# Kernel optimization log

Hardware: AMD Instinct MI355X
Metric: run time of the kernel (lower is better)

Reference implementation:

```python
import jax, jax.numpy as jnp
import numpy as np

HEAD_DIM = 64  # d_model // n_heads = 1024 // 16

def setup_inputs() -> dict:
    key = jax.random.key(0)
    k1, k2, k3, k4, k5 = jax.random.split(key, 5)
    B, H, S, D = 4, 16, 1024, HEAD_DIM
    return {
        "q": jax.random.normal(k1, (B, H, S, D), dtype=jnp.float32),
        "k": jax.random.normal(k2, (B, H, D, S), dtype=jnp.float32),
        "v": jax.random.normal(k3, (B, H, S, D), dtype=jnp.float32),
        "prev": jax.random.normal(k4, (B, H, S, S), dtype=jnp.float32),
        "attn_mask": jax.random.normal(k5, (1, 1, S, S), dtype=jnp.float32),
        "scale": jnp.asarray(HEAD_DIM ** (-0.5), dtype=jnp.float32),
    }

def reference(q, k, v, prev, attn_mask, scale):
    # scores: [B, H, S, S]; k is pre-transposed to [B, H, D, S]
    attn_scores = jnp.einsum('bhsd,bhdt->bhst', q, k) * scale
    attn_scores = attn_scores + prev + attn_mask  # additive float mask branch
    attn_weights = jax.nn.softmax(attn_scores, axis=-1)
    # dropout p=0.0 -> identity
    output = jnp.einsum('bhst,bhtd->bhsd', attn_weights, v)
    # res_attention=True -> return scores too
    return (output, attn_weights, attn_scores)
```

## Files before the change

### kernel.cpp

```cpp
#include <hip/hip_runtime.h>

#define S 1024
#define D 64
#define R 16
#define BH 64
#define SUBP 68

typedef float v4f __attribute__((ext_vector_type(4)));

__global__ __launch_bounds__(256, 4)
void attn_fused_kernel(const float* __restrict__ q,
                       const float* __restrict__ k,
                       const float* __restrict__ v,
                       const float* __restrict__ prev,
                       const float* __restrict__ mask,
                       const float* __restrict__ scale_p,
                       float* __restrict__ out,
                       float* __restrict__ weights,
                       float* __restrict__ scores)
{
    __shared__ float q_lds[R][D];
    __shared__ float s_sub[4][R][SUBP];
    __shared__ float red_max[4][R];
    __shared__ float red_sum[4][R];

    const int tile = blockIdx.x;
    const int bh   = blockIdx.y;
    const int tid  = (int)threadIdx.x;
    const int lane = tid & 63;
    const int wid  = tid >> 6;
    const int r0   = tile * R;

    const float* qb = q    + (size_t)bh * S * D + (size_t)r0 * D;
    const float* kb = k    + (size_t)bh * D * S;
    const float* vb = v    + (size_t)bh * S * D;
    const float* pb = prev + (size_t)bh * S * S + (size_t)r0 * S;
    const float* mb = mask + (size_t)r0 * S;
    float* wout = weights + (size_t)bh * S * S + (size_t)r0 * S;
    float* sout = scores  + (size_t)bh * S * S + (size_t)r0 * S;
    float* oout = out     + (size_t)bh * S * D + (size_t)r0 * D;

    const float scale  = *scale_p;
    const float rscale = 1.0f / scale;

    {
        float4 qv = *(const float4*)(qb + (size_t)tid * 4);
        *(float4*)&q_lds[tid >> 4][(tid & 15) * 4] = qv;
    }
    __syncthreads();

    const int t0 = tid * 4;
    float acc[R][4];

#pragma unroll
    for (int r = 0; r < R; ++r) {
        v4f p4 = __builtin_nontemporal_load((const v4f*)(pb + (size_t)r * S + t0));
        v4f m4 = *(const v4f*)(mb + (size_t)r * S + t0);
        acc[r][0] = (p4[0] + m4[0]) * rscale;
        acc[r][1] = (p4[1] + m4[1]) * rscale;
        acc[r][2] = (p4[2] + m4[2]) * rscale;
        acc[r][3] = (p4[3] + m4[3]) * rscale;
    }

#pragma unroll 2
    for (int kk = 0; kk < D / 4; ++kk) {
        const float* kp = kb + (size_t)(kk * 4) * S + t0;
        float4 k0 = *(const float4*)(kp);
        float4 k1 = *(const float4*)(kp + S);
        float4 k2 = *(const float4*)(kp + 2 * S);
        float4 k3 = *(const float4*)(kp + 3 * S);
#pragma unroll
        for (int r = 0; r < R; ++r) {
            float4 q4 = *(const float4*)&q_lds[r][kk * 4];
            acc[r][0] = fmaf(q4.w, k3.x, fmaf(q4.z, k2.x, fmaf(q4.y, k1.x, fmaf(q4.x, k0.x, acc[r][0]))));
            acc[r][1] = fmaf(q4.w, k3.y, fmaf(q4.z, k2.y, fmaf(q4.y, k1.y, fmaf(q4.x, k0.y, acc[r][1]))));
            acc[r][2] = fmaf(q4.w, k3.z, fmaf(q4.z, k2.z, fmaf(q4.y, k1.z, fmaf(q4.x, k0.z, acc[r][2]))));
            acc[r][3] = fmaf(q4.w, k3.w, fmaf(q4.z, k2.w, fmaf(q4.y, k1.w, fmaf(q4.x, k0.w, acc[r][3]))));
        }
    }

#pragma unroll
    for (int r = 0; r < R; ++r) {
        acc[r][0] *= scale; acc[r][1] *= scale; acc[r][2] *= scale; acc[r][3] *= scale;
        v4f s4v = { acc[r][0], acc[r][1], acc[r][2], acc[r][3] };
        __builtin_nontemporal_store(s4v, (v4f*)(sout + (size_t)r * S + t0));
    }

    {
        float rmax[R];
#pragma unroll
        for (int r = 0; r < R; ++r) {
            float m = fmaxf(fmaxf(acc[r][0], acc[r][1]), fmaxf(acc[r][2], acc[r][3]));
#pragma unroll
            for (int off = 32; off > 0; off >>= 1)
                m = fmaxf(m, __shfl_xor(m, off));
            rmax[r] = m;
        }
        if (lane == 0) {
#pragma unroll
            for (int r = 0; r < R; ++r) red_max[wid][r] = rmax[r];
        }
    }
    __syncthreads();

    {
        float rsum[R];
#pragma unroll
        for (int r = 0; r < R; ++r) {
            float gm = fmaxf(fmaxf(red_max[0][r], red_max[1][r]),
                             fmaxf(red_max[2][r], red_max[3][r]));
            acc[r][0] = __expf(acc[r][0] - gm);
            acc[r][1] = __expf(acc[r][1] - gm);
            acc[r][2] = __expf(acc[r][2] - gm);
            acc[r][3] = __expf(acc[r][3] - gm);
            float ssum = (acc[r][0] + acc[r][1]) + (acc[r][2] + acc[r][3]);
#pragma unroll
            for (int off = 32; off > 0; off >>= 1)
                ssum += __shfl_xor(ssum, off);
            rsum[r] = ssum;
        }
        if (lane == 0) {
#pragma unroll
            for (int r = 0; r < R; ++r) red_sum[wid][r] = rsum[r];
        }
    }
    __syncthreads();

#pragma unroll
    for (int r = 0; r < R; ++r) {
        float gs = (red_sum[0][r] + red_sum[1][r]) + (red_sum[2][r] + red_sum[3][r]);
        float inv = 1.0f / gs;
        acc[r][0] *= inv; acc[r][1] *= inv; acc[r][2] *= inv; acc[r][3] *= inv;
        v4f w4v = { acc[r][0], acc[r][1], acc[r][2], acc[r][3] };
        __builtin_nontemporal_store(w4v, (v4f*)(wout + (size_t)r * S + t0));
    }

    const int g0 = lane >> 4;
    const int dq = lane & 15;
    const float* vw = vb + (size_t)(wid * 256) * D;

    float4 p0 = {0.f,0.f,0.f,0.f};
    float4 p1 = {0.f,0.f,0.f,0.f};
    float4 p2 = {0.f,0.f,0.f,0.f};
    float4 p3 = {0.f,0.f,0.f,0.f};

#pragma unroll 1
    for (int s4 = 0; s4 < 4; ++s4) {
        asm volatile("" ::: "memory");
        if (g0 == s4) {
#pragma unroll
            for (int r = 0; r < R; ++r) {
                float4 w4 = { acc[r][0], acc[r][1], acc[r][2], acc[r][3] };
                *(float4*)&s_sub[wid][r][dq * 4] = w4;
            }
        }
        asm volatile("s_waitcnt lgkmcnt(0)" ::: "memory");

        const float* vs = vw + (size_t)(s4 * 64) * D;
#pragma unroll 2
        for (int j = 0; j < 16; ++j) {
            float4 w0 = *(const float4*)&s_sub[wid][g0     ][j * 4];
            float4 w1 = *(const float4*)&s_sub[wid][g0 + 4 ][j * 4];
            float4 w2 = *(const float4*)&s_sub[wid][g0 + 8 ][j * 4];
            float4 w3 = *(const float4*)&s_sub[wid][g0 + 12][j * 4];
            const float* vp = vs + (size_t)(j * 4) * D + dq * 4;
            float4 v0 = *(const float4*)(vp);
            float4 v1 = *(const float4*)(vp + D);
            float4 v2 = *(const float4*)(vp + 2 * D);
            float4 v3 = *(const float4*)(vp + 3 * D);
            p0.x = fmaf(w0.w, v3.x, fmaf(w0.z, v2.x, fmaf(w0.y, v1.x, fmaf(w0.x, v0.x, p0.x))));
            p0.y = fmaf(w0.w, v3.y, fmaf(w0.z, v2.y, fmaf(w0.y, v1.y, fmaf(w0.x, v0.y, p0.y))));
            p0.z = fmaf(w0.w, v3.z, fmaf(w0.z, v2.z, fmaf(w0.y, v1.z, fmaf(w0.x, v0.z, p0.z))));
            p0.w = fmaf(w0.w, v3.w, fmaf(w0.z, v2.w, fmaf(w0.y, v1.w, fmaf(w0.x, v0.w, p0.w))));
            p1.x = fmaf(w1.w, v3.x, fmaf(w1.z, v2.x, fmaf(w1.y, v1.x, fmaf(w1.x, v0.x, p1.x))));
            p1.y = fmaf(w1.w, v3.y, fmaf(w1.z, v2.y, fmaf(w1.y, v1.y, fmaf(w1.x, v0.y, p1.y))));
            p1.z = fmaf(w1.w, v3.z, fmaf(w1.z, v2.z, fmaf(w1.y, v1.z, fmaf(w1.x, v0.z, p1.z))));
            p1.w = fmaf(w1.w, v3.w, fmaf(w1.z, v2.w, fmaf(w1.y, v1.w, fmaf(w1.x, v0.w, p1.w))));
            p2.x = fmaf(w2.w, v3.x, fmaf(w2.z, v2.x, fmaf(w2.y, v1.x, fmaf(w2.x, v0.x, p2.x))));
            p2.y = fmaf(w2.w, v3.y, fmaf(w2.z, v2.y, fmaf(w2.y, v1.y, fmaf(w2.x, v0.y, p2.y))));
            p2.z = fmaf(w2.w, v3.z, fmaf(w2.z, v2.z, fmaf(w2.y, v1.z, fmaf(w2.x, v0.z, p2.z))));
            p2.w = fmaf(w2.w, v3.w, fmaf(w2.z, v2.w, fmaf(w2.y, v1.w, fmaf(w2.x, v0.w, p2.w))));
            p3.x = fmaf(w3.w, v3.x, fmaf(w3.z, v2.x, fmaf(w3.y, v1.x, fmaf(w3.x, v0.x, p3.x))));
            p3.y = fmaf(w3.w, v3.y, fmaf(w3.z, v2.y, fmaf(w3.y, v1.y, fmaf(w3.x, v0.y, p3.y))));
            p3.z = fmaf(w3.w, v3.z, fmaf(w3.z, v2.z, fmaf(w3.y, v1.z, fmaf(w3.x, v0.z, p3.z))));
            p3.w = fmaf(w3.w, v3.w, fmaf(w3.z, v2.w, fmaf(w3.y, v1.w, fmaf(w3.x, v0.w, p3.w))));
        }
    }

    asm volatile("" ::: "memory");
    *(float4*)&s_sub[wid][g0     ][dq * 4] = p0;
    *(float4*)&s_sub[wid][g0 + 4 ][dq * 4] = p1;
    *(float4*)&s_sub[wid][g0 + 8 ][dq * 4] = p2;
    *(float4*)&s_sub[wid][g0 + 12][dq * 4] = p3;
    __syncthreads();
    {
        const int row = tid >> 4;
        const int dq2 = tid & 15;
        float4 a0 = *(const float4*)&s_sub[0][row][dq2 * 4];
        float4 a1 = *(const float4*)&s_sub[1][row][dq2 * 4];
        float4 a2 = *(const float4*)&s_sub[2][row][dq2 * 4];
        float4 a3 = *(const float4*)&s_sub[3][row][dq2 * 4];
        v4f o;
        o[0] = (a0.x + a1.x) + (a2.x + a3.x);
        o[1] = (a0.y + a1.y) + (a2.y + a3.y);
        o[2] = (a0.z + a1.z) + (a2.z + a3.z);
        o[3] = (a0.w + a1.w) + (a2.w + a3.w);
        __builtin_nontemporal_store(o, (v4f*)(oout + (size_t)row * D + dq2 * 4));
    }
}

extern "C" void kernel_launch(void* const* d_in, const int* in_sizes, int n_in,
                              void* d_out, int out_size, void* d_ws, size_t ws_size,
                              hipStream_t stream) {
    (void)in_sizes; (void)n_in; (void)out_size; (void)d_ws; (void)ws_size;
    const float* q     = (const float*)d_in[0];
    const float* k     = (const float*)d_in[1];
    const float* v     = (const float*)d_in[2];
    const float* prev  = (const float*)d_in[3];
    const float* mask  = (const float*)d_in[4];
    const float* scale = (const float*)d_in[5];

    float* out     = (float*)d_out;
    float* weights = out + (size_t)4 * 16 * 1024 * 64;
    float* scores  = weights + (size_t)4 * 16 * 1024 * 1024;

    dim3 grid(S / R, BH);
    attn_fused_kernel<<<grid, 256, 0, stream>>>(q, k, v, prev, mask, scale,
                                                out, weights, scores);
}
```

Before: 377.3 us.

## Halve rows per block and overlap prev/mask loads with the QK loop

Rows per block drop from 16 to 8, with the launch-bounds occupancy hint lowered from 4 to 3, so each thread holds half as many score accumulators and the grid has twice as many blocks. The prev and mask loads move out of a separate prologue and into the first eight iterations of the QK^T loop, so their latency overlaps the K loads and FMAs. The scale and additive bias are then applied afterwards with a single fma per element. The cost is that every K and V tile is now re-read by twice as many blocks, which doubles L2/HBM traffic for those operands.

Result: slower. 430.4 us (+14.1%).

```diff
diff --git a/kernel.cpp b/kernel.cpp
--- a/kernel.cpp
+++ b/kernel.cpp
@@ -2,13 +2,13 @@
 
 #define S 1024
 #define D 64
-#define R 16
+#define R 8
 #define BH 64
 #define SUBP 68
 
 typedef float v4f __attribute__((ext_vector_type(4)));
 
-__global__ __launch_bounds__(256, 4)
+__global__ __launch_bounds__(256, 3)
 void attn_fused_kernel(const float* __restrict__ q,
                        const float* __restrict__ k,
                        const float* __restrict__ v,
@@ -40,10 +40,7 @@
     float* sout = scores  + (size_t)bh * S * S + (size_t)r0 * S;
     float* oout = out     + (size_t)bh * S * D + (size_t)r0 * D;
 
-    const float scale  = *scale_p;
-    const float rscale = 1.0f / scale;
-
-    {
+    if (tid < 128) {
         float4 qv = *(const float4*)(qb + (size_t)tid * 4);
         *(float4*)&q_lds[tid >> 4][(tid & 15) * 4] = qv;
     }
@@ -51,24 +48,22 @@
 
     const int t0 = tid * 4;
     float acc[R][4];
-
 #pragma unroll
     for (int r = 0; r < R; ++r) {
-        v4f p4 = __builtin_nontemporal_load((const v4f*)(pb + (size_t)r * S + t0));
-        v4f m4 = *(const v4f*)(mb + (size_t)r * S + t0);
-        acc[r][0] = (p4[0] + m4[0]) * rscale;
-        acc[r][1] = (p4[1] + m4[1]) * rscale;
-        acc[r][2] = (p4[2] + m4[2]) * rscale;
-        acc[r][3] = (p4[3] + m4[3]) * rscale;
-    }
-
-#pragma unroll 2
-    for (int kk = 0; kk < D / 4; ++kk) {
+        acc[r][0] = 0.f; acc[r][1] = 0.f; acc[r][2] = 0.f; acc[r][3] = 0.f;
+    }
+
+    v4f pbuf[R], mbuf[R];
+
+#pragma unroll
+    for (int kk = 0; kk < 8; ++kk) {
         const float* kp = kb + (size_t)(kk * 4) * S + t0;
         float4 k0 = *(const float4*)(kp);
         float4 k1 = *(const float4*)(kp + S);
         float4 k2 = *(const float4*)(kp + 2 * S);
         float4 k3 = *(const float4*)(kp + 3 * S);
+        pbuf[kk] = __builtin_nontemporal_load((const v4f*)(pb + (size_t)kk * S + t0));
+        mbuf[kk] = *(const v4f*)(mb + (size_t)kk * S + t0);
 #pragma unroll
         for (int r = 0; r < R; ++r) {
             float4 q4 = *(const float4*)&q_lds[r][kk * 4];
@@ -79,9 +74,34 @@
         }
     }
 
+#pragma unroll 2
+    for (int kk = 8; kk < 16; ++kk) {
+        const float* kp = kb + (size_t)(kk * 4) * S + t0;
+        float4 k0 = *(const float4*)(kp);
+        float4 k1 = *(const float4*)(kp + S);
+        float4 k2 = *(const float4*)(kp + 2 * S);
+        float4 k3 = *(const float4*)(kp + 3 * S);
+#pragma unroll
+        for (int r = 0; r < R; ++r) {
+            float4 q4 = *(const float4*)&q_lds[r][kk * 4];
+            acc[r][0] = fmaf(q4.w, k3.x, fmaf(q4.z, k2.x, fmaf(q4.y, k1.x, fmaf(q4.x, k0.x, acc[r][0]))));
+            acc[r][1] = fmaf(q4.w, k3.y, fmaf(q4.z, k2.y, fmaf(q4.y, k1.y, fmaf(q4.x, k0.y, acc[r][1]))));
+            acc[r][2] = fmaf(q4.w, k3.z, fmaf(q4.z, k2.z, fmaf(q4.y, k1.z, fmaf(q4.x, k0.z, acc[r][2]))));
+            acc[r][3] = fmaf(q4.w, k3.w, fmaf(q4.z, k2.w, fmaf(q4.y, k1.w, fmaf(q4.x, k0.w, acc[r][3]))));
+        }
+    }
+
+    const float scale = *scale_p;
 #pragma unroll
     for (int r = 0; r < R; ++r) {
-        acc[r][0] *= scale; acc[r][1] *= scale; acc[r][2] *= scale; acc[r][3] *= scale;
+        float b0 = pbuf[r][0] + mbuf[r][0];
+        float b1 = pbuf[r][1] + mbuf[r][1];
+        float b2 = pbuf[r][2] + mbuf[r][2];
+        float b3 = pbuf[r][3] + mbuf[r][3];
+        acc[r][0] = fmaf(acc[r][0], scale, b0);
+        acc[r][1] = fmaf(acc[r][1], scale, b1);
+        acc[r][2] = fmaf(acc[r][2], scale, b2);
+        acc[r][3] = fmaf(acc[r][3], scale, b3);
         v4f s4v = { acc[r][0], acc[r][1], acc[r][2], acc[r][3] };
         __builtin_nontemporal_store(s4v, (v4f*)(sout + (size_t)r * S + t0));
     }
@@ -141,8 +161,6 @@
 
     float4 p0 = {0.f,0.f,0.f,0.f};
     float4 p1 = {0.f,0.f,0.f,0.f};
-    float4 p2 = {0.f,0.f,0.f,0.f};
-    float4 p3 = {0.f,0.f,0.f,0.f};
 
 #pragma unroll 1
     for (int s4 = 0; s4 < 4; ++s4) {
@@ -159,10 +177,8 @@
         const float* vs = vw + (size_t)(s4 * 64) * D;
 #pragma unroll 2
         for (int j = 0; j < 16; ++j) {
-            float4 w0 = *(const float4*)&s_sub[wid][g0     ][j * 4];
-            float4 w1 = *(const float4*)&s_sub[wid][g0 + 4 ][j * 4];
-            float4 w2 = *(const float4*)&s_sub[wid][g0 + 8 ][j * 4];
-            float4 w3 = *(const float4*)&s_sub[wid][g0 + 12][j * 4];
+            float4 w0 = *(const float4*)&s_sub[wid][g0    ][j * 4];
+            float4 w1 = *(const float4*)&s_sub[wid][g0 + 4][j * 4];
             const float* vp = vs + (size_t)(j * 4) * D + dq * 4;
             float4 v0 = *(const float4*)(vp);
             float4 v1 = *(const float4*)(vp + D);
@@ -176,24 +192,14 @@
             p1.y = fmaf(w1.w, v3.y, fmaf(w1.z, v2.y, fmaf(w1.y, v1.y, fmaf(w1.x, v0.y, p1.y))));
             p1.z = fmaf(w1.w, v3.z, fmaf(w1.z, v2.z, fmaf(w1.y, v1.z, fmaf(w1.x, v0.z, p1.z))));
             p1.w = fmaf(w1.w, v3.w, fmaf(w1.z, v2.w, fmaf(w1.y, v1.w, fmaf(w1.x, v0.w, p1.w))));
-            p2.x = fmaf(w2.w, v3.x, fmaf(w2.z, v2.x, fmaf(w2.y, v1.x, fmaf(w2.x, v0.x, p2.x))));
-            p2.y = fmaf(w2.w, v3.y, fmaf(w2.z, v2.y, fmaf(w2.y, v1.y, fmaf(w2.x, v0.y, p2.y))));
-            p2.z = fmaf(w2.w, v3.z, fmaf(w2.z, v2.z, fmaf(w2.y, v1.z, fmaf(w2.x, v0.z, p2.z))));
-            p2.w = fmaf(w2.w, v3.w, fmaf(w2.z, v2.w, fmaf(w2.y, v1.w, fmaf(w2.x, v0.w, p2.w))));
-            p3.x = fmaf(w3.w, v3.x, fmaf(w3.z, v2.x, fmaf(w3.y, v1.x, fmaf(w3.x, v0.x, p3.x))));
-            p3.y = fmaf(w3.w, v3.y, fmaf(w3.z, v2.y, fmaf(w3.y, v1.y, fmaf(w3.x, v0.y, p3.y))));
-            p3.z = fmaf(w3.w, v3.z, fmaf(w3.z, v2.z, fmaf(w3.y, v1.z, fmaf(w3.x, v0.z, p3.z))));
-            p3.w = fmaf(w3.w, v3.w, fmaf(w3.z, v2.w, fmaf(w3.y, v1.w, fmaf(w3.x, v0.w, p3.w))));
         }
     }
 
     asm volatile("" ::: "memory");
-    *(float4*)&s_sub[wid][g0     ][dq * 4] = p0;
-    *(float4*)&s_sub[wid][g0 + 4 ][dq * 4] = p1;
-    *(float4*)&s_sub[wid][g0 + 8 ][dq * 4] = p2;
-    *(float4*)&s_sub[wid][g0 + 12][dq * 4] = p3;
-    __syncthreads();
-    {
+    *(float4*)&s_sub[wid][g0    ][dq * 4] = p0;
+    *(float4*)&s_sub[wid][g0 + 4][dq * 4] = p1;
+    __syncthreads();
+    if (tid < 128) {
         const int row = tid >> 4;
         const int dq2 = tid & 15;
         float4 a0 = *(const float4*)&s_sub[0][row][dq2 * 4];
```
